# Performance work log

Hardware: AMD Instinct MI355X
Metric: run time of the kernel (lower is better)

Reference implementation:

```python
import jax, jax.numpy as jnp
import numpy as np

B, N, D = 2048, 64, 256  # batch, n_linears, n_in == n_out
N_RECURS = 3             # loop runs n_recurs + 1 = 4 times


def _make_masks():
    # per-group active block sizes in [128, 256], mimicking _init_masks
    n_act = np.minimum(128 + 32 * (np.arange(N) % 5), D)  # [N]
    col = np.arange(D)
    active = col[None, :] < n_act[:, None]                 # [N, D]
    w_mask = (active[:, :, None] & active[:, None, :]).astype(np.float32)  # [N, D, D]
    b_mask = active.astype(np.float32)                     # [N, D]
    return jnp.asarray(w_mask), jnp.asarray(b_mask)


def setup_inputs() -> dict:
    key = jax.random.key(0)
    k1, k2, k3 = jax.random.split(key, 3)
    x = jax.random.normal(k1, (B, N, D), dtype=jnp.float32)
    # kaiming_uniform-like scale for fan_in = D
    bound = 1.0 / np.sqrt(D)
    weights = jax.random.uniform(k2, (N, D, D), dtype=jnp.float32, minval=-bound, maxval=bound)
    biases = jax.random.uniform(k3, (N, D), dtype=jnp.float32, minval=-bound, maxval=bound)
    weight_mask, bias_mask = _make_masks()
    return {"x": x, "weights": weights, "biases": biases,
            "weight_mask": weight_mask, "bias_mask": bias_mask}


def reference(x, weights, biases, weight_mask, bias_mask):
    # Mask is static across recurrence steps; torch code recomputes it each
    # step but the values are identical, so hoist (same math).
    w = weights * weight_mask          # [N, D, D]
    b = (biases * bias_mask)[None]     # [1, N, D]
    for _ in range(N_RECURS + 1):
        # grouped small GEMM: x[b,n,i] @ w[n,j,i]^T -> [b,n,j]
        x = x + jax.nn.relu(jnp.einsum('bni,nji->bnj', x, w) + b)
    return x
```

## Files before the change

kernel.cpp:

```cpp
#include <hip/hip_runtime.h>
#include <hip/hip_bf16.h>
#include <cstdint>
#include <cstddef>

#define B_TOT   2048
#define N_LIN   64
#define D_DIM   256
#define NSTEPS  4
#define BT      64

typedef __attribute__((ext_vector_type(8))) short short8;
typedef __attribute__((ext_vector_type(4))) float f32x4;

__device__ __forceinline__ void split2(float f, unsigned short& h, unsigned short& l) {
    unsigned u = __float_as_uint(f);
    unsigned r = u + 0x7FFFu + ((u >> 16) & 1u);
    h = (unsigned short)(r >> 16);
    float hf = __uint_as_float(r & 0xFFFF0000u);
    float rem = f - hf;
    unsigned u2 = __float_as_uint(rem);
    unsigned r2 = u2 + 0x7FFFu + ((u2 >> 16) & 1u);
    l = (unsigned short)(r2 >> 16);
}

__device__ __forceinline__ float bf16_to_f(unsigned short s) {
    return __uint_as_float((unsigned)s << 16);
}

__global__ void prep_kernel(const float* __restrict__ w, const float* __restrict__ wm,
                            unsigned short* __restrict__ w_hi,
                            unsigned short* __restrict__ w_lo) {
    const int nW4 = N_LIN * D_DIM * D_DIM / 4;
    int stride = gridDim.x * blockDim.x;
    for (int i = blockIdx.x * blockDim.x + threadIdx.x; i < nW4; i += stride) {
        float4 wv = ((const float4*)w)[i];
        float4 mv = ((const float4*)wm)[i];
        ushort4 h, l;
        split2(wv.x * mv.x, h.x, l.x);
        split2(wv.y * mv.y, h.y, l.y);
        split2(wv.z * mv.z, h.z, l.z);
        split2(wv.w * mv.w, h.w, l.w);
        ((ushort4*)w_hi)[i] = h;
        ((ushort4*)w_lo)[i] = l;
    }
}

template <bool ONFLY>
__global__ __launch_bounds__(512, 4)
void fused_kernel(const float* __restrict__ xin,
                  const unsigned short* __restrict__ w_hi,
                  const unsigned short* __restrict__ w_lo,
                  const float* __restrict__ wraw,
                  const float* __restrict__ wmask,
                  const float* __restrict__ braw,
                  const float* __restrict__ bmask,
                  float* __restrict__ xout) {
    __shared__ unsigned short xh[BT * 256];
    __shared__ unsigned short xl[BT * 256];
    __shared__ int s_cnt[4];

    const int tid  = threadIdx.x;
    const int lane = tid & 63;
    const int wvid = tid >> 6;
    const int quad = lane >> 4;
    const int l16  = lane & 15;

    const int xcd = blockIdx.x & 7;
    const int j8  = blockIdx.x >> 3;
    const int n   = (xcd << 3) | (j8 & 7);
    const int btk = j8 >> 3;

    const size_t row_stride = (size_t)N_LIN * D_DIM;
    const float* xsrc = xin  + ((size_t)btk * BT * N_LIN + n) * D_DIM;
    float*       xdst = xout + ((size_t)btk * BT * N_LIN + n) * D_DIM;

    for (int i = tid; i < BT * (D_DIM / 4); i += 512) {
        int r = i >> 6, c4 = i & 63;
        float4 v = ((const float4*)(xsrc + (size_t)r * row_stride))[c4];
        ushort4 h, l;
        split2(v.x, h.x, l.x);
        split2(v.y, h.y, l.y);
        split2(v.z, h.z, l.z);
        split2(v.w, h.w, l.w);
        int pi = r * 256 + ((((c4 >> 1) ^ (r & 7))) << 3) + ((c4 & 1) << 2);
        *((ushort4*)&xh[pi]) = h;
        *((ushort4*)&xl[pi]) = l;
    }

    if (wvid < 4) {
        float bv = bmask[n * D_DIM + wvid * 64 + lane];
        unsigned long long actm = __ballot(bv != 0.0f);
        if (lane == 0) s_cnt[wvid] = __popcll(actm);
    }

    float bias_r[2][4];
    #pragma unroll
    for (int u = 0; u < 2; ++u)
        #pragma unroll
        for (int rg = 0; rg < 4; ++rg) {
            int c = (wvid + 8 * u) * 16 + quad * 4 + rg;
            bias_r[u][rg] = braw[n * D_DIM + c] * bmask[n * D_DIM + c];
        }

    float bmj[2];
    if (ONFLY) {
        #pragma unroll
        for (int u = 0; u < 2; ++u)
            bmj[u] = bmask[n * D_DIM + (wvid + 8 * u) * 16 + l16];
    }

    const size_t wbase = ((size_t)n * D_DIM + (size_t)wvid * 16 + l16) * D_DIM + (size_t)quad * 8;
    const size_t ustride = (size_t)128 * D_DIM;

    __syncthreads();

    const int n_act  = s_cnt[0] + s_cnt[1] + s_cnt[2] + s_cnt[3];
    const int kt_lim = n_act >> 5;
    const int njt    = n_act >> 4;
    const bool u1a   = (wvid + 8) < njt;

    short8 whA[2], wlA[2], whB[2], wlB[2];

    auto loadW = [&](int kt, short8* h, short8* l) {
        size_t off = wbase + (size_t)(kt << 5);
        h[0] = *((const short8*)(w_hi + off));
        l[0] = *((const short8*)(w_lo + off));
        if (u1a) {
            h[1] = *((const short8*)(w_hi + off + ustride));
            l[1] = *((const short8*)(w_lo + off + ustride));
        }
    };

    if (!ONFLY) loadW(0, whA, wlA);

    #pragma unroll 1
    for (int step = 0; step < NSTEPS; ++step) {
        f32x4 acc[2][4];
        #pragma unroll
        for (int u = 0; u < 2; ++u)
            #pragma unroll
            for (int bt = 0; bt < 4; ++bt)
                acc[u][bt] = f32x4{0.f, 0.f, 0.f, 0.f};

        auto compute = [&](int kt, const short8* wh, const short8* wl) {
            const int c0 = kt * 32 + quad * 8;
            #pragma unroll
            for (int bt = 0; bt < 4; ++bt) {
                int m  = bt * 16 + l16;
                int pi = m * 256 + ((((c0 >> 3) ^ (m & 7))) << 3);
                short8 x8h = *((const short8*)&xh[pi]);
                short8 x8l = *((const short8*)&xl[pi]);
                acc[0][bt] = __builtin_amdgcn_mfma_f32_16x16x32_bf16(wh[0], x8h, acc[0][bt], 0, 0, 0);
                acc[0][bt] = __builtin_amdgcn_mfma_f32_16x16x32_bf16(wh[0], x8l, acc[0][bt], 0, 0, 0);
                acc[0][bt] = __builtin_amdgcn_mfma_f32_16x16x32_bf16(wl[0], x8h, acc[0][bt], 0, 0, 0);
                if (u1a) {
                    acc[1][bt] = __builtin_amdgcn_mfma_f32_16x16x32_bf16(wh[1], x8h, acc[1][bt], 0, 0, 0);
                    acc[1][bt] = __builtin_amdgcn_mfma_f32_16x16x32_bf16(wh[1], x8l, acc[1][bt], 0, 0, 0);
                    acc[1][bt] = __builtin_amdgcn_mfma_f32_16x16x32_bf16(wl[1], x8h, acc[1][bt], 0, 0, 0);
                }
            }
        };

        if (!ONFLY) {
            int kt = 0;
            for (; kt + 2 <= kt_lim; kt += 2) {
                loadW(kt + 1, whB, wlB);
                compute(kt, whA, wlA);
                int k2 = kt + 2;
                loadW(k2 < kt_lim ? k2 : kt + 1, whA, wlA);
                compute(kt + 1, whB, wlB);
            }
            if (kt < kt_lim) compute(kt, whA, wlA);
            loadW(0, whA, wlA);
        } else {
            for (int kt = 0; kt < kt_lim; ++kt) {
                const float* bmi_p = bmask + n * D_DIM + kt * 32 + quad * 8;
                float4 mi0 = ((const float4*)bmi_p)[0];
                float4 mi1 = ((const float4*)bmi_p)[1];
                float mi[8] = {mi0.x, mi0.y, mi0.z, mi0.w, mi1.x, mi1.y, mi1.z, mi1.w};
                #pragma unroll
                for (int u = 0; u < 2; ++u) if (u == 0 || u1a) {
                    const float* wp = wraw + wbase + (size_t)u * ustride + (size_t)(kt << 5);
                    float4 w0 = ((const float4*)wp)[0];
                    float4 w1 = ((const float4*)wp)[1];
                    float wvv[8] = {w0.x, w0.y, w0.z, w0.w, w1.x, w1.y, w1.z, w1.w};
                    #pragma unroll
                    for (int j = 0; j < 8; ++j) {
                        unsigned short h, l;
                        split2(wvv[j] * bmj[u] * mi[j], h, l);
                        whA[u][j] = (short)h;
                        wlA[u][j] = (short)l;
                    }
                }
                compute(kt, whA, wlA);
            }
        }

        __syncthreads();

        const bool last = (step == NSTEPS - 1);
        #pragma unroll
        for (int u = 0; u < 2; ++u) {
            const bool act = (u == 0) || u1a;
            if (act || last) {
                #pragma unroll
                for (int bt = 0; bt < 4; ++bt) {
                    int r  = bt * 16 + l16;
                    int c0 = (wvid + 8 * u) * 16 + quad * 4;
                    int pi = r * 256 + ((((c0 >> 3) ^ (r & 7))) << 3) + (c0 & 7);
                    ushort4 oh = *((const ushort4*)&xh[pi]);
                    ushort4 ol = *((const ushort4*)&xl[pi]);
                    float xn[4];
                    xn[0] = bf16_to_f(oh.x) + bf16_to_f(ol.x);
                    xn[1] = bf16_to_f(oh.y) + bf16_to_f(ol.y);
                    xn[2] = bf16_to_f(oh.z) + bf16_to_f(ol.z);
                    xn[3] = bf16_to_f(oh.w) + bf16_to_f(ol.w);
                    if (act) {
                        #pragma unroll
                        for (int rg = 0; rg < 4; ++rg)
                            xn[rg] += fmaxf(acc[u][bt][rg] + bias_r[u][rg], 0.f);
                    }
                    if (last) {
                        float4 o;
                        o.x = xn[0]; o.y = xn[1]; o.z = xn[2]; o.w = xn[3];
                        *((float4*)(xdst + (size_t)r * row_stride + c0)) = o;
                    } else if (act) {
                        ushort4 h, l;
                        split2(xn[0], h.x, l.x);
                        split2(xn[1], h.y, l.y);
                        split2(xn[2], h.z, l.z);
                        split2(xn[3], h.w, l.w);
                        *((ushort4*)&xh[pi]) = h;
                        *((ushort4*)&xl[pi]) = l;
                    }
                }
            }
        }
        __syncthreads();
    }
}

extern "C" void kernel_launch(void* const* d_in, const int* in_sizes, int n_in,
                              void* d_out, int out_size, void* d_ws, size_t ws_size,
                              hipStream_t stream) {
    const float* x  = (const float*)d_in[0];
    const float* w  = (const float*)d_in[1];
    const float* b  = (const float*)d_in[2];
    const float* wm = (const float*)d_in[3];
    const float* bm = (const float*)d_in[4];
    float* out = (float*)d_out;

    const size_t needW = (size_t)2 * N_LIN * D_DIM * D_DIM * sizeof(unsigned short);
    const int grid = (B_TOT / BT) * N_LIN;

    if (ws_size >= needW) {
        unsigned short* w_hi = (unsigned short*)d_ws;
        unsigned short* w_lo = w_hi + (size_t)N_LIN * D_DIM * D_DIM;
        prep_kernel<<<1024, 256, 0, stream>>>(w, wm, w_hi, w_lo);
        fused_kernel<false><<<grid, 512, 0, stream>>>(x, w_hi, w_lo, w, wm, b, bm, out);
    } else {
        fused_kernel<true><<<grid, 512, 0, stream>>>(x, nullptr, nullptr, w, wm, b, bm, out);
    }
}
```

Baseline: 477.8 us.

## Halve batch tile, keep residual in registers, fold bias into accumulator init

Shrinks the per-block batch tile from 64 to 32 rows, doubling the grid, and raises the launch-bounds occupancy target to 8 blocks. The fp32 residual now stays in registers across steps instead of being rebuilt from the LDS hi/lo pair. The bias is staged in shared memory and used as the initial accumulator value. The explicit weight double-buffer prefetch is dropped in favour of a simple unrolled loop. The x split now truncates the high half instead of rounding it, and the final barrier is skipped. Smaller tiles mean each weight tile is reused across fewer rows and more weight traffic overall, and the tighter register budget risks spills.

```diff
diff --git a/kernel.cpp b/kernel.cpp
--- a/kernel.cpp
+++ b/kernel.cpp
@@ -7,7 +7,7 @@
 #define N_LIN   64
 #define D_DIM   256
 #define NSTEPS  4
-#define BT      64
+#define BT      32
 
 typedef __attribute__((ext_vector_type(8))) short short8;
 typedef __attribute__((ext_vector_type(4))) float f32x4;
@@ -18,6 +18,15 @@
     h = (unsigned short)(r >> 16);
     float hf = __uint_as_float(r & 0xFFFF0000u);
     float rem = f - hf;
+    unsigned u2 = __float_as_uint(rem);
+    unsigned r2 = u2 + 0x7FFFu + ((u2 >> 16) & 1u);
+    l = (unsigned short)(r2 >> 16);
+}
+
+__device__ __forceinline__ void split2t(float f, unsigned short& h, unsigned short& l) {
+    unsigned u = __float_as_uint(f);
+    h = (unsigned short)(u >> 16);
+    float rem = f - __uint_as_float(u & 0xFFFF0000u);
     unsigned u2 = __float_as_uint(rem);
     unsigned r2 = u2 + 0x7FFFu + ((u2 >> 16) & 1u);
     l = (unsigned short)(r2 >> 16);
@@ -46,7 +55,7 @@
 }
 
 template <bool ONFLY>
-__global__ __launch_bounds__(512, 4)
+__global__ __launch_bounds__(512, 8)
 void fused_kernel(const float* __restrict__ xin,
                   const unsigned short* __restrict__ w_hi,
                   const unsigned short* __restrict__ w_lo,
@@ -57,6 +66,7 @@
                   float* __restrict__ xout) {
     __shared__ unsigned short xh[BT * 256];
     __shared__ unsigned short xl[BT * 256];
+    __shared__ float s_bias[D_DIM];
     __shared__ int s_cnt[4];
 
     const int tid  = threadIdx.x;
@@ -78,29 +88,22 @@
         int r = i >> 6, c4 = i & 63;
         float4 v = ((const float4*)(xsrc + (size_t)r * row_stride))[c4];
         ushort4 h, l;
-        split2(v.x, h.x, l.x);
-        split2(v.y, h.y, l.y);
-        split2(v.z, h.z, l.z);
-        split2(v.w, h.w, l.w);
+        split2t(v.x, h.x, l.x);
+        split2t(v.y, h.y, l.y);
+        split2t(v.z, h.z, l.z);
+        split2t(v.w, h.w, l.w);
         int pi = r * 256 + ((((c4 >> 1) ^ (r & 7))) << 3) + ((c4 & 1) << 2);
         *((ushort4*)&xh[pi]) = h;
         *((ushort4*)&xl[pi]) = l;
     }
+
+    if (tid < D_DIM) s_bias[tid] = braw[n * D_DIM + tid] * bmask[n * D_DIM + tid];
 
     if (wvid < 4) {
         float bv = bmask[n * D_DIM + wvid * 64 + lane];
         unsigned long long actm = __ballot(bv != 0.0f);
         if (lane == 0) s_cnt[wvid] = __popcll(actm);
     }
-
-    float bias_r[2][4];
-    #pragma unroll
-    for (int u = 0; u < 2; ++u)
-        #pragma unroll
-        for (int rg = 0; rg < 4; ++rg) {
-            int c = (wvid + 8 * u) * 16 + quad * 4 + rg;
-            bias_r[u][rg] = braw[n * D_DIM + c] * bmask[n * D_DIM + c];
-        }
 
     float bmj[2];
     if (ONFLY) {
@@ -119,80 +122,82 @@
     const int njt    = n_act >> 4;
     const bool u1a   = (wvid + 8) < njt;
 
-    short8 whA[2], wlA[2], whB[2], wlB[2];
-
-    auto loadW = [&](int kt, short8* h, short8* l) {
-        size_t off = wbase + (size_t)(kt << 5);
-        h[0] = *((const short8*)(w_hi + off));
-        l[0] = *((const short8*)(w_lo + off));
-        if (u1a) {
-            h[1] = *((const short8*)(w_hi + off + ustride));
-            l[1] = *((const short8*)(w_lo + off + ustride));
-        }
-    };
-
-    if (!ONFLY) loadW(0, whA, wlA);
+    float xr[2][2][4];
+    #pragma unroll
+    for (int u = 0; u < 2; ++u)
+        #pragma unroll
+        for (int bt = 0; bt < 2; ++bt) {
+            int r  = bt * 16 + l16;
+            int c0 = (wvid + 8 * u) * 16 + quad * 4;
+            int pi = r * 256 + ((((c0 >> 3) ^ (r & 7))) << 3) + (c0 & 7);
+            ushort4 oh = *((const ushort4*)&xh[pi]);
+            ushort4 ol = *((const ushort4*)&xl[pi]);
+            xr[u][bt][0] = bf16_to_f(oh.x) + bf16_to_f(ol.x);
+            xr[u][bt][1] = bf16_to_f(oh.y) + bf16_to_f(ol.y);
+            xr[u][bt][2] = bf16_to_f(oh.z) + bf16_to_f(ol.z);
+            xr[u][bt][3] = bf16_to_f(oh.w) + bf16_to_f(ol.w);
+        }
 
     #pragma unroll 1
     for (int step = 0; step < NSTEPS; ++step) {
-        f32x4 acc[2][4];
-        #pragma unroll
-        for (int u = 0; u < 2; ++u)
-            #pragma unroll
-            for (int bt = 0; bt < 4; ++bt)
-                acc[u][bt] = f32x4{0.f, 0.f, 0.f, 0.f};
-
-        auto compute = [&](int kt, const short8* wh, const short8* wl) {
-            const int c0 = kt * 32 + quad * 8;
-            #pragma unroll
-            for (int bt = 0; bt < 4; ++bt) {
-                int m  = bt * 16 + l16;
-                int pi = m * 256 + ((((c0 >> 3) ^ (m & 7))) << 3);
-                short8 x8h = *((const short8*)&xh[pi]);
-                short8 x8l = *((const short8*)&xl[pi]);
-                acc[0][bt] = __builtin_amdgcn_mfma_f32_16x16x32_bf16(wh[0], x8h, acc[0][bt], 0, 0, 0);
-                acc[0][bt] = __builtin_amdgcn_mfma_f32_16x16x32_bf16(wh[0], x8l, acc[0][bt], 0, 0, 0);
-                acc[0][bt] = __builtin_amdgcn_mfma_f32_16x16x32_bf16(wl[0], x8h, acc[0][bt], 0, 0, 0);
+        f32x4 acc[2][2];
+        {
+            f32x4 bv0 = *((const f32x4*)&s_bias[wvid * 16 + quad * 4]);
+            f32x4 bv1 = *((const f32x4*)&s_bias[wvid * 16 + 128 + quad * 4]);
+            acc[0][0] = bv0; acc[0][1] = bv0;
+            acc[1][0] = bv1; acc[1][1] = bv1;
+        }
+
+        #pragma unroll 2
+        for (int kt = 0; kt < kt_lim; ++kt) {
+            short8 wh0, wl0, wh1, wl1;
+            if (!ONFLY) {
+                size_t off = wbase + (size_t)(kt << 5);
+                wh0 = *((const short8*)(w_hi + off));
+                wl0 = *((const short8*)(w_lo + off));
                 if (u1a) {
-                    acc[1][bt] = __builtin_amdgcn_mfma_f32_16x16x32_bf16(wh[1], x8h, acc[1][bt], 0, 0, 0);
-                    acc[1][bt] = __builtin_amdgcn_mfma_f32_16x16x32_bf16(wh[1], x8l, acc[1][bt], 0, 0, 0);
-                    acc[1][bt] = __builtin_amdgcn_mfma_f32_16x16x32_bf16(wl[1], x8h, acc[1][bt], 0, 0, 0);
-                }
-            }
-        };
-
-        if (!ONFLY) {
-            int kt = 0;
-            for (; kt + 2 <= kt_lim; kt += 2) {
-                loadW(kt + 1, whB, wlB);
-                compute(kt, whA, wlA);
-                int k2 = kt + 2;
-                loadW(k2 < kt_lim ? k2 : kt + 1, whA, wlA);
-                compute(kt + 1, whB, wlB);
-            }
-            if (kt < kt_lim) compute(kt, whA, wlA);
-            loadW(0, whA, wlA);
-        } else {
-            for (int kt = 0; kt < kt_lim; ++kt) {
+                    wh1 = *((const short8*)(w_hi + off + ustride));
+                    wl1 = *((const short8*)(w_lo + off + ustride));
+                }
+            } else {
                 const float* bmi_p = bmask + n * D_DIM + kt * 32 + quad * 8;
                 float4 mi0 = ((const float4*)bmi_p)[0];
                 float4 mi1 = ((const float4*)bmi_p)[1];
                 float mi[8] = {mi0.x, mi0.y, mi0.z, mi0.w, mi1.x, mi1.y, mi1.z, mi1.w};
                 #pragma unroll
-                for (int u = 0; u < 2; ++u) if (u == 0 || u1a) {
+                for (int u = 0; u < 2; ++u) {
+                    if (u == 1 && !u1a) break;
                     const float* wp = wraw + wbase + (size_t)u * ustride + (size_t)(kt << 5);
                     float4 w0 = ((const float4*)wp)[0];
                     float4 w1 = ((const float4*)wp)[1];
                     float wvv[8] = {w0.x, w0.y, w0.z, w0.w, w1.x, w1.y, w1.z, w1.w};
+                    short8 th, tl;
                     #pragma unroll
                     for (int j = 0; j < 8; ++j) {
                         unsigned short h, l;
-                        split2(wvv[j] * bmj[u] * mi[j], h, l);
-                        whA[u][j] = (short)h;
-                        wlA[u][j] = (short)l;
+                        split2t(wvv[j] * bmj[u] * mi[j], h, l);
+                        th[j] = (short)h;
+                        tl[j] = (short)l;
                     }
-                }
-                compute(kt, whA, wlA);
+                    if (u == 0) { wh0 = th; wl0 = tl; }
+                    else        { wh1 = th; wl1 = tl; }
+                }
+            }
+            const int c0 = kt * 32 + quad * 8;
+            #pragma unroll
+            for (int bt = 0; bt < 2; ++bt) {
+                int m  = bt * 16 + l16;
+                int pi = m * 256 + ((((c0 >> 3) ^ (m & 7))) << 3);
+                short8 x8h = *((const short8*)&xh[pi]);
+                short8 x8l = *((const short8*)&xl[pi]);
+                acc[0][bt] = __builtin_amdgcn_mfma_f32_16x16x32_bf16(wh0, x8h, acc[0][bt], 0, 0, 0);
+                acc[0][bt] = __builtin_amdgcn_mfma_f32_16x16x32_bf16(wh0, x8l, acc[0][bt], 0, 0, 0);
+                acc[0][bt] = __builtin_amdgcn_mfma_f32_16x16x32_bf16(wl0, x8h, acc[0][bt], 0, 0, 0);
+                if (u1a) {
+                    acc[1][bt] = __builtin_amdgcn_mfma_f32_16x16x32_bf16(wh1, x8h, acc[1][bt], 0, 0, 0);
+                    acc[1][bt] = __builtin_amdgcn_mfma_f32_16x16x32_bf16(wh1, x8l, acc[1][bt], 0, 0, 0);
+                    acc[1][bt] = __builtin_amdgcn_mfma_f32_16x16x32_bf16(wl1, x8h, acc[1][bt], 0, 0, 0);
+                }
             }
         }
 
@@ -202,41 +207,31 @@
         #pragma unroll
         for (int u = 0; u < 2; ++u) {
             const bool act = (u == 0) || u1a;
-            if (act || last) {
+            #pragma unroll
+            for (int bt = 0; bt < 2; ++bt) {
+                int r  = bt * 16 + l16;
+                int c0 = (wvid + 8 * u) * 16 + quad * 4;
                 #pragma unroll
-                for (int bt = 0; bt < 4; ++bt) {
-                    int r  = bt * 16 + l16;
-                    int c0 = (wvid + 8 * u) * 16 + quad * 4;
+                for (int rg = 0; rg < 4; ++rg)
+                    xr[u][bt][rg] += fmaxf(acc[u][bt][rg], 0.f);
+                if (last) {
+                    float4 o;
+                    o.x = xr[u][bt][0]; o.y = xr[u][bt][1];
+                    o.z = xr[u][bt][2]; o.w = xr[u][bt][3];
+                    *((float4*)(xdst + (size_t)r * row_stride + c0)) = o;
+                } else if (act) {
                     int pi = r * 256 + ((((c0 >> 3) ^ (r & 7))) << 3) + (c0 & 7);
-                    ushort4 oh = *((const ushort4*)&xh[pi]);
-                    ushort4 ol = *((const ushort4*)&xl[pi]);
-                    float xn[4];
-                    xn[0] = bf16_to_f(oh.x) + bf16_to_f(ol.x);
-                    xn[1] = bf16_to_f(oh.y) + bf16_to_f(ol.y);
-                    xn[2] = bf16_to_f(oh.z) + bf16_to_f(ol.z);
-                    xn[3] = bf16_to_f(oh.w) + bf16_to_f(ol.w);
-                    if (act) {
-                        #pragma unroll
-                        for (int rg = 0; rg < 4; ++rg)
-                            xn[rg] += fmaxf(acc[u][bt][rg] + bias_r[u][rg], 0.f);
-                    }
-                    if (last) {
-                        float4 o;
-                        o.x = xn[0]; o.y = xn[1]; o.z = xn[2]; o.w = xn[3];
-                        *((float4*)(xdst + (size_t)r * row_stride + c0)) = o;
-                    } else if (act) {
-                        ushort4 h, l;
-                        split2(xn[0], h.x, l.x);
-                        split2(xn[1], h.y, l.y);
-                        split2(xn[2], h.z, l.z);
-                        split2(xn[3], h.w, l.w);
-                        *((ushort4*)&xh[pi]) = h;
-                        *((ushort4*)&xl[pi]) = l;
-                    }
+                    ushort4 h, l;
+                    split2t(xr[u][bt][0], h.x, l.x);
+                    split2t(xr[u][bt][1], h.y, l.y);
+                    split2t(xr[u][bt][2], h.z, l.z);
+                    split2t(xr[u][bt][3], h.w, l.w);
+                    *((ushort4*)&xh[pi]) = h;
+                    *((ushort4*)&xl[pi]) = l;
                 }
             }
         }
-        __syncthreads();
+        if (!last) __syncthreads();
     }
 }
 
```

Result: slower. 679.4 us (+42.2%).
